# Kernel optimization log

Measured on AMD Instinct MI355X. Metric: run time of the kernel, lower is better.

## Reference

```python
import jax, jax.numpy as jnp
import numpy as np

D_MODEL = 1024
NUM_HEADS = 16
ENERGY_SCALE = 0.1
LN_EPS = 1e-5


def layernorm(x, gamma, beta):
    mu = jnp.mean(x, axis=-1, keepdims=True)
    var = jnp.var(x, axis=-1, keepdims=True)
    return (x - mu) * jax.lax.rsqrt(var + LN_EPS) * gamma + beta


def setup_inputs() -> dict:
    key = jax.random.key(0)
    ks = jax.random.split(key, 8)
    B, L, D = 2, 2048, D_MODEL
    s = 0.02
    return {
        "x": jax.random.normal(ks[0], (B, L, D), dtype=jnp.float32),
        "wq": jax.random.normal(ks[1], (D, D), dtype=jnp.float32) * s,
        "wk": jax.random.normal(ks[2], (D, D), dtype=jnp.float32) * s,
        "wv": jax.random.normal(ks[3], (D, D), dtype=jnp.float32) * s,
        "wo_w": jax.random.normal(ks[4], (D, D), dtype=jnp.float32) * s,
        "wo_b": jnp.zeros((D,), dtype=jnp.float32),
        "ep_w": jax.random.normal(ks[5], (D, D), dtype=jnp.float32) * s,
        "ep_b": jnp.zeros((D,), dtype=jnp.float32),
        "en_g": jnp.ones((D,), dtype=jnp.float32),
        "en_b": jnp.zeros((D,), dtype=jnp.float32),
        "ln_g": jnp.ones((D,), dtype=jnp.float32),
        "ln_b": jnp.zeros((D,), dtype=jnp.float32),
    }


def reference(x, wq, wk, wv, wo_w, wo_b, ep_w, ep_b, en_g, en_b, ln_g, ln_b):
    B, L, D = x.shape
    H, dk = NUM_HEADS, D // NUM_HEADS
    # Linear projections (torch convention: y = x @ W^T), split heads -> [B,H,L,dk]
    q = (x @ wq.T).reshape(B, L, H, dk).transpose(0, 2, 1, 3)
    k = (x @ wk.T).reshape(B, L, H, dk).transpose(0, 2, 1, 3)
    v = (x @ wv.T).reshape(B, L, H, dk).transpose(0, 2, 1, 3)
    scores = jnp.einsum("bhld,bhmd->bhlm", q, k) / jnp.sqrt(jnp.float32(dk))
    # Energy bias: ef @ ef^T as a proper GEMM (same math as the broadcast-mul-sum)
    ef = layernorm(x @ ep_w.T + ep_b, en_g, en_b)
    energy_bias = jnp.einsum("bld,bmd->blm", ef, ef)  # [B,L,L]
    scores = scores + ENERGY_SCALE * energy_bias[:, None, :, :]
    attn = jax.nn.softmax(scores, axis=-1)  # dropout is identity in eval mode
    ctx = jnp.einsum("bhlm,bhmd->bhld", attn, v)
    ctx = ctx.transpose(0, 2, 1, 3).reshape(B, L, D)
    out = ctx @ wo_w.T + wo_b
    return layernorm(out + x, ln_g, ln_b), attn
```

## Files before the change

kernel.cpp:

```cpp
#include <hip/hip_runtime.h>
#include <math.h>

#define D_MODEL 1024
#define NUM_HEADS 16
#define DK 64
#define L_SEQ 2048
#define BATCH 2
#define LN_EPS 1e-5f
#define ENERGY_SCALE 0.1f

typedef __attribute__((ext_vector_type(8))) short short8;
typedef __attribute__((ext_vector_type(4))) float f32x4;
typedef __attribute__((address_space(1))) const unsigned int gas_u32;
typedef __attribute__((address_space(3))) unsigned int las_u32;

__device__ __forceinline__ float waveReduceSum(float v) {
#pragma unroll
    for (int off = 32; off > 0; off >>= 1) v += __shfl_xor(v, off, 64);
    return v;
}

__device__ __forceinline__ unsigned short f2bf(float f) {
    unsigned int u = __float_as_uint(f);
    u += 0x7fff + ((u >> 16) & 1);
    return (unsigned short)(u >> 16);
}
__device__ __forceinline__ float bf2f(unsigned short u) {
    return __uint_as_float((unsigned int)u << 16);
}

__global__ __launch_bounds__(256) void cvt6(
    const float* s0, const float* s1, const float* s2,
    const float* s3, const float* s4, const float* s5,
    unsigned short* d0, unsigned short* d1, unsigned short* d2,
    unsigned short* d3, unsigned short* d4, unsigned short* d5,
    long long n0, long long n1, long long n2, long long n3, long long n4, long long n5)
{
    const float* s; unsigned short* d; long long n;
    switch (blockIdx.y) {
        case 0: s = s0; d = d0; n = n0; break;
        case 1: s = s1; d = d1; n = n1; break;
        case 2: s = s2; d = d2; n = n2; break;
        case 3: s = s3; d = d3; n = n3; break;
        case 4: s = s4; d = d4; n = n4; break;
        default: s = s5; d = d5; n = n5; break;
    }
    long long i = ((long long)blockIdx.x * 256 + threadIdx.x) * 4;
    if (i >= n) return;
    float4 v = *(const float4*)(s + i);
    ushort4 o;
    o.x = f2bf(v.x); o.y = f2bf(v.y); o.z = f2bf(v.z); o.w = f2bf(v.w);
    *(ushort4*)(d + i) = o;
}

__global__ __launch_bounds__(256) void gemm_bf16(
    const unsigned short* __restrict__ A, const unsigned short* __restrict__ B,
    const float* __restrict__ bias, float* __restrict__ Cf, unsigned short* __restrict__ Ch,
    int N, int K, long long sA, long long sB, long long sC)
{
    A += (long long)blockIdx.z * sA;
    B += (long long)blockIdx.z * sB;
    __shared__ unsigned short As[128 * 64];
    __shared__ unsigned short Bs[128 * 64];
    const int tid = threadIdx.x;
    const int lane = tid & 63, w = tid >> 6;
    const int quad = lane >> 4, col = lane & 15;
    const int wm = w & 1, wn = w >> 1;
    const int row0 = blockIdx.y * 128, col0 = blockIdx.x * 128;

    const int lr = lane >> 3, lc = lane & 7;
    const int gcs = (lc ^ lr) * 8;

    f32x4 acc[4][4];
#pragma unroll
    for (int mt = 0; mt < 4; mt++)
#pragma unroll
        for (int nt = 0; nt < 4; nt++) acc[mt][nt] = (f32x4){0.f, 0.f, 0.f, 0.f};

    for (int k0 = 0; k0 < K; k0 += 64) {
        __syncthreads();
#pragma unroll
        for (int p = 0; p < 4; p++) {
            const int rb = w * 32 + p * 8;
            __builtin_amdgcn_global_load_lds(
                (gas_u32*)(A + (long long)(row0 + rb + lr) * K + k0 + gcs),
                (las_u32*)(As + rb * 64), 16, 0, 0);
            __builtin_amdgcn_global_load_lds(
                (gas_u32*)(B + (long long)(col0 + rb + lr) * K + k0 + gcs),
                (las_u32*)(Bs + rb * 64), 16, 0, 0);
        }
        __syncthreads();
#pragma unroll
        for (int kc = 0; kc < 2; kc++) {
            const int csw = ((quad + 4 * kc) ^ (col & 7)) * 8;
            short8 af[4], bfr[4];
#pragma unroll
            for (int mt = 0; mt < 4; mt++)
                af[mt] = *(const short8*)(As + (wm * 64 + mt * 16 + col) * 64 + csw);
#pragma unroll
            for (int nt = 0; nt < 4; nt++)
                bfr[nt] = *(const short8*)(Bs + (wn * 64 + nt * 16 + col) * 64 + csw);
#pragma unroll
            for (int mt = 0; mt < 4; mt++)
#pragma unroll
                for (int nt = 0; nt < 4; nt++)
                    acc[mt][nt] = __builtin_amdgcn_mfma_f32_16x16x32_bf16(af[mt], bfr[nt], acc[mt][nt], 0, 0, 0);
        }
    }

#pragma unroll
    for (int mt = 0; mt < 4; mt++)
#pragma unroll
        for (int nt = 0; nt < 4; nt++)
#pragma unroll
            for (int reg = 0; reg < 4; reg++) {
                long long row = row0 + wm * 64 + mt * 16 + quad * 4 + reg;
                int c = col0 + wn * 64 + nt * 16 + col;
                float v = acc[mt][nt][reg];
                if (bias) v += bias[c];
                if (Cf) Cf[blockIdx.z * sC + row * N + c] = v;
                else    Ch[blockIdx.z * sC + row * N + c] = f2bf(v);
            }
}

__global__ __launch_bounds__(256) void proj_gemm(
    const unsigned short* __restrict__ Xh,
    const unsigned short* __restrict__ wqh, const unsigned short* __restrict__ wkh,
    const unsigned short* __restrict__ wvh, const unsigned short* __restrict__ eph,
    const float* __restrict__ ep_b,
    unsigned short* __restrict__ Qh, unsigned short* __restrict__ Kh,
    unsigned short* __restrict__ Vf, float* __restrict__ EP)
{
    const unsigned short* B;
    switch (blockIdx.z) {
        case 0: B = wqh; break;
        case 1: B = wkh; break;
        case 2: B = wvh; break;
        default: B = eph; break;
    }
    __shared__ unsigned short As[128 * 64];
    __shared__ unsigned short Bs[128 * 64];
    const int tid = threadIdx.x;
    const int lane = tid & 63, w = tid >> 6;
    const int quad = lane >> 4, col = lane & 15;
    const int wm = w & 1, wn = w >> 1;
    const int row0 = blockIdx.y * 128, col0 = blockIdx.x * 128;
    const int K = D_MODEL, N = D_MODEL;

    const int lr = lane >> 3, lc = lane & 7;
    const int gcs = (lc ^ lr) * 8;

    f32x4 acc[4][4];
#pragma unroll
    for (int mt = 0; mt < 4; mt++)
#pragma unroll
        for (int nt = 0; nt < 4; nt++) acc[mt][nt] = (f32x4){0.f, 0.f, 0.f, 0.f};

    for (int k0 = 0; k0 < K; k0 += 64) {
        __syncthreads();
#pragma unroll
        for (int p = 0; p < 4; p++) {
            const int rb = w * 32 + p * 8;
            __builtin_amdgcn_global_load_lds(
                (gas_u32*)(Xh + (long long)(row0 + rb + lr) * K + k0 + gcs),
                (las_u32*)(As + rb * 64), 16, 0, 0);
            __builtin_amdgcn_global_load_lds(
                (gas_u32*)(B + (long long)(col0 + rb + lr) * K + k0 + gcs),
                (las_u32*)(Bs + rb * 64), 16, 0, 0);
        }
        __syncthreads();
#pragma unroll
        for (int kc = 0; kc < 2; kc++) {
            const int csw = ((quad + 4 * kc) ^ (col & 7)) * 8;
            short8 af[4], bfr[4];
#pragma unroll
            for (int mt = 0; mt < 4; mt++)
                af[mt] = *(const short8*)(As + (wm * 64 + mt * 16 + col) * 64 + csw);
#pragma unroll
            for (int nt = 0; nt < 4; nt++)
                bfr[nt] = *(const short8*)(Bs + (wn * 64 + nt * 16 + col) * 64 + csw);
#pragma unroll
            for (int mt = 0; mt < 4; mt++)
#pragma unroll
                for (int nt = 0; nt < 4; nt++)
                    acc[mt][nt] = __builtin_amdgcn_mfma_f32_16x16x32_bf16(af[mt], bfr[nt], acc[mt][nt], 0, 0, 0);
        }
    }

    unsigned short* Hout = (blockIdx.z == 0) ? Qh : (blockIdx.z == 1) ? Kh : Vf;
#pragma unroll
    for (int mt = 0; mt < 4; mt++)
#pragma unroll
        for (int nt = 0; nt < 4; nt++)
#pragma unroll
            for (int reg = 0; reg < 4; reg++) {
                long long row = row0 + wm * 64 + mt * 16 + quad * 4 + reg;
                int c = col0 + wn * 64 + nt * 16 + col;
                float v = acc[mt][nt][reg];
                if (blockIdx.z == 3) EP[row * N + c] = v + ep_b[c];
                else                 Hout[row * N + c] = f2bf(v);
            }
}

__global__ __launch_bounds__(256) void ln_rows(
    const float* __restrict__ in, const float* __restrict__ res,
    const float* __restrict__ g, const float* __restrict__ bta,
    float* __restrict__ outf, unsigned short* __restrict__ outh)
{
    const long long row = blockIdx.x;
    const float* ip = in + row * D_MODEL;
    const float* rp = res ? res + row * D_MODEL : nullptr;
    const int tid = threadIdx.x;
    float vals[4];
    float s = 0.f, ss = 0.f;
#pragma unroll
    for (int j = 0; j < 4; j++) {
        int idx = tid + j * 256;
        float v = ip[idx];
        if (rp) v += rp[idx];
        vals[j] = v; s += v; ss += v * v;
    }
    __shared__ float sred[4], ssred[4];
    s = waveReduceSum(s); ss = waveReduceSum(ss);
    int wave = tid >> 6, lane = tid & 63;
    if (lane == 0) { sred[wave] = s; ssred[wave] = ss; }
    __syncthreads();
    float ts = sred[0] + sred[1] + sred[2] + sred[3];
    float tss = ssred[0] + ssred[1] + ssred[2] + ssred[3];
    float mu = ts * (1.f / D_MODEL);
    float var = tss * (1.f / D_MODEL) - mu * mu;
    float rs = rsqrtf(var + LN_EPS);
#pragma unroll
    for (int j = 0; j < 4; j++) {
        int idx = tid + j * 256;
        float o = (vals[j] - mu) * rs * g[idx] + bta[idx];
        if (outf) outf[row * D_MODEL + idx] = o;
        else      outh[row * D_MODEL + idx] = f2bf(o);
    }
}

__global__ __launch_bounds__(256) void transpose_v(
    const unsigned short* __restrict__ V, unsigned short* __restrict__ Vt)
{
    const int m0 = blockIdx.x * 64, h = blockIdx.y, b = blockIdx.z;
    __shared__ unsigned int t[64][65];
    const int tid = threadIdx.x;
    {
        int r = tid >> 4, c4 = (tid & 15) * 4;
#pragma unroll
        for (int i = 0; i < 4; i++) {
            int row = r + i * 16;
            ushort4 v = *(const ushort4*)(V + ((long long)b * L_SEQ + m0 + row) * D_MODEL + h * DK + c4);
            t[row][c4] = v.x; t[row][c4 + 1] = v.y; t[row][c4 + 2] = v.z; t[row][c4 + 3] = v.w;
        }
    }
    __syncthreads();
    const int lane = tid & 63, wv = tid >> 6;
#pragma unroll
    for (int i = 0; i < 16; i++) {
        int d = wv * 16 + i;
        Vt[(((long long)(b * NUM_HEADS + h)) * DK + d) * L_SEQ + m0 + lane] = (unsigned short)t[lane][d];
    }
}

__global__ __launch_bounds__(256) void eb_stats(
    const float* __restrict__ EB, float* __restrict__ ebmax, float* __restrict__ ebtmax)
{
    const long long row = blockIdx.x;
    const float* p = EB + row * L_SEQ;
    const int tid = threadIdx.x;
    float4 a = *(const float4*)(p + tid * 8);
    float4 c = *(const float4*)(p + tid * 8 + 4);
    float m = fmaxf(fmaxf(fmaxf(a.x, a.y), fmaxf(a.z, a.w)),
                    fmaxf(fmaxf(c.x, c.y), fmaxf(c.z, c.w)));
    m = fmaxf(m, __shfl_xor(m, 1, 64));
    m = fmaxf(m, __shfl_xor(m, 2, 64));
    m = fmaxf(m, __shfl_xor(m, 4, 64));
    if ((tid & 7) == 0) ebtmax[row * 32 + (tid >> 3)] = m;
    m = fmaxf(m, __shfl_xor(m, 8, 64));
    m = fmaxf(m, __shfl_xor(m, 16, 64));
    m = fmaxf(m, __shfl_xor(m, 32, 64));
    __shared__ float red[4];
    if ((tid & 63) == 0) red[tid >> 6] = m;
    __syncthreads();
    if (tid == 0)
        ebmax[row] = fmaxf(fmaxf(red[0], red[1]), fmaxf(red[2], red[3]));
}

__global__ __launch_bounds__(256) void qk_stats(
    const unsigned short* __restrict__ Qh, const unsigned short* __restrict__ Kh,
    float* __restrict__ qn, float* __restrict__ kn)
{
    const int l0 = blockIdx.x * 64, h = blockIdx.y, b = blockIdx.z;
    const int tid = threadIdx.x;
    const int r = tid >> 2, p4 = (tid & 3) * 16;
    const unsigned short* q = Qh + ((long long)b * L_SEQ + l0 + r) * D_MODEL + h * DK + p4;
    const unsigned short* k = Kh + ((long long)b * L_SEQ + l0 + r) * D_MODEL + h * DK + p4;
    float sq = 0.f, sk = 0.f;
#pragma unroll
    for (int i = 0; i < 16; i++) {
        float qv = bf2f(q[i]); sq += qv * qv;
        float kv = bf2f(k[i]); sk += kv * kv;
    }
    sq += __shfl_xor(sq, 1, 64); sq += __shfl_xor(sq, 2, 64);
    sk += __shfl_xor(sk, 1, 64); sk += __shfl_xor(sk, 2, 64);
    if ((tid & 3) == 0) {
        long long idx = ((long long)(b * NUM_HEADS + h)) * L_SEQ + l0 + r;
        qn[idx] = sqrtf(sq);
        kn[idx] = sqrtf(sk);
    }
}

__global__ __launch_bounds__(256) void kstats2(
    const float* __restrict__ kn, float* __restrict__ kmax, float* __restrict__ ktmax)
{
    const long long bh = blockIdx.x;
    const float* p = kn + bh * L_SEQ;
    const int tid = threadIdx.x;
    float4 a = *(const float4*)(p + tid * 8);
    float4 c = *(const float4*)(p + tid * 8 + 4);
    float m = fmaxf(fmaxf(fmaxf(a.x, a.y), fmaxf(a.z, a.w)),
                    fmaxf(fmaxf(c.x, c.y), fmaxf(c.z, c.w)));
    m = fmaxf(m, __shfl_xor(m, 1, 64));
    m = fmaxf(m, __shfl_xor(m, 2, 64));
    m = fmaxf(m, __shfl_xor(m, 4, 64));
    if ((tid & 7) == 0) ktmax[bh * 32 + (tid >> 3)] = m;
    m = fmaxf(m, __shfl_xor(m, 8, 64));
    m = fmaxf(m, __shfl_xor(m, 16, 64));
    m = fmaxf(m, __shfl_xor(m, 32, 64));
    __shared__ float red[4];
    if ((tid & 63) == 0) red[tid >> 6] = m;
    __syncthreads();
    if (tid == 0)
        kmax[bh] = fmaxf(fmaxf(red[0], red[1]), fmaxf(red[2], red[3]));
}

__global__ __launch_bounds__(64) void skip_mask(
    const float* __restrict__ ebmax, const float* __restrict__ ebtmax,
    const float* __restrict__ qn, const float* __restrict__ kmax,
    const float* __restrict__ ktmax, unsigned int* __restrict__ skipm)
{
    const int l0 = blockIdx.x * 64, h = blockIdx.y, b = blockIdx.z;
    const int tid = threadIdx.x;
    const int row = l0 + tid;
    const int bh = b * NUM_HEADS + h;
    float q = qn[(long long)bh * L_SEQ + row];
    float Mh = ENERGY_SCALE * ebmax[(long long)b * L_SEQ + row] + q * kmax[bh] * 0.125f + 0.02f;
    const float* ebt = ebtmax + ((long long)b * L_SEQ + row) * 32;
    const float* ktm = ktmax + bh * 32;
    unsigned int m = 0;
    for (int t = 0; t < 32; t++) {
        float ub = ENERGY_SCALE * ebt[t] + q * ktm[t] * 0.125f;
        unsigned long long bal = __ballot(ub < Mh - 45.0f);
        if (bal == ~0ull) m |= (1u << t);
    }
    if (tid == 0) skipm[bh * 32 + blockIdx.x] = m;
}

__global__ __launch_bounds__(256) void attn_mfma(
    const unsigned short* __restrict__ Qh, const unsigned short* __restrict__ Kh,
    const unsigned short* __restrict__ Vt, const float* __restrict__ EB,
    const float* __restrict__ ebmax, const float* __restrict__ qn,
    const float* __restrict__ kmax, const unsigned int* __restrict__ skipm,
    float* __restrict__ attn_out, unsigned short* __restrict__ CTXh)
{
    __shared__ unsigned short Ks[2][64 * 64];
    __shared__ unsigned short Vts[64 * 64];
    __shared__ unsigned short Ps[4 * 16 * 72];

    const int tid = threadIdx.x;
    const int lane = tid & 63, w = tid >> 6;
    const int quad = lane >> 4, col = lane & 15;
    const int l0 = blockIdx.x * 64;
    const int h = blockIdx.y, b = blockIdx.z;

    const unsigned int sm = skipm[(b * NUM_HEADS + h) * 32 + blockIdx.x];

    const unsigned short* kbase = Kh + ((long long)b * L_SEQ) * D_MODEL + h * DK;
    const unsigned short* vbase = Vt + ((long long)(b * NUM_HEADS + h)) * DK * L_SEQ;

    const int lr = lane >> 3, lc = lane & 7;
    const int gsw = (lc ^ lr) * 8;

    auto nxt = [&](int t) -> int {
        unsigned int rem = ~sm;
        if (t >= 0) rem &= (t >= 31) ? 0u : (0xFFFFFFFFu << (t + 1));
        return rem ? (int)__builtin_ctz(rem) : -1;
    };
    const int t0 = nxt(-1);

    if (t0 >= 0) {
#pragma unroll
        for (int p = 0; p < 2; p++) {
            const int rb = w * 8 + p * 32;
            __builtin_amdgcn_global_load_lds(
                (gas_u32*)(kbase + (long long)(t0 * 64 + rb + lr) * D_MODEL + gsw),
                (las_u32*)(&Ks[0][rb * 64]), 16, 0, 0);
        }
    }

    {
        float* zbase = attn_out + (((long long)(b * NUM_HEADS + h)) * L_SEQ + l0) * L_SEQ;
        const int zc = (tid & 15) * 4;
        const int zr = tid >> 4;
        const float4 zv = {0.f, 0.f, 0.f, 0.f};
        for (int t = 0; t < 32; t++) {
            if (!(sm & (1u << t))) continue;
            float* tb = zbase + t * 64 + zc;
#pragma unroll
            for (int rr = 0; rr < 4; rr++)
                *(float4*)(tb + (long long)(rr * 16 + zr) * L_SEQ) = zv;
        }
    }

    short8 aq[2];
    {
        const unsigned short* qrow = Qh + ((long long)b * L_SEQ + l0 + w * 16 + col) * D_MODEL + h * DK;
        aq[0] = *(const short8*)(qrow + quad * 8);
        aq[1] = *(const short8*)(qrow + 32 + quad * 8);
    }

    float Mhat[4];
    {
        const float km = kmax[b * NUM_HEADS + h];
#pragma unroll
        for (int reg = 0; reg < 4; reg++) {
            int row = l0 + w * 16 + quad * 4 + reg;
            float qb = qn[((long long)(b * NUM_HEADS + h)) * L_SEQ + row];
            Mhat[reg] = ENERGY_SCALE * ebmax[(long long)b * L_SEQ + row] +
                        qb * km * 0.125f + 0.02f;
        }
    }

    const float* ebp = EB + ((long long)b * L_SEQ + l0 + w * 16 + quad * 4) * L_SEQ + col;

    __syncthreads();

    float rowSacc[4] = {0.f, 0.f, 0.f, 0.f};
    int cur = 0;
    for (int t = t0; t >= 0; ) {
        const int tn = nxt(t);
        if (tn >= 0) {
#pragma unroll
            for (int p = 0; p < 2; p++) {
                const int rb = w * 8 + p * 32;
                __builtin_amdgcn_global_load_lds(
                    (gas_u32*)(kbase + (long long)(tn * 64 + rb + lr) * D_MODEL + gsw),
                    (las_u32*)(&Ks[cur ^ 1][rb * 64]), 16, 0, 0);
            }
        }
        const int m0 = t * 64;

        f32x4 acc[4];
#pragma unroll
        for (int nt = 0; nt < 4; nt++) acc[nt] = (f32x4){0.f, 0.f, 0.f, 0.f};
        __builtin_amdgcn_s_setprio(1);
#pragma unroll
        for (int nt = 0; nt < 4; nt++)
#pragma unroll
            for (int kc = 0; kc < 2; kc++) {
                short8 bk = *(const short8*)(&Ks[cur][((nt * 16 + col) << 6) +
                                                     (((quad + 4 * kc) ^ (col & 7)) << 3)]);
                acc[nt] = __builtin_amdgcn_mfma_f32_16x16x32_bf16(aq[kc], bk, acc[nt], 0, 0, 0);
            }
        __builtin_amdgcn_s_setprio(0);
#pragma unroll
        for (int nt = 0; nt < 4; nt++)
#pragma unroll
            for (int reg = 0; reg < 4; reg++) {
                float s = acc[nt][reg] * 0.125f + ENERGY_SCALE * ebp[(long long)reg * L_SEQ + m0 + nt * 16];
                rowSacc[reg] += __expf(s - Mhat[reg]);
            }
        __syncthreads();
        cur ^= 1;
        t = tn;
    }

    float invS[4];
#pragma unroll
    for (int reg = 0; reg < 4; reg++) {
        float v = rowSacc[reg];
#pragma unroll
        for (int off = 8; off > 0; off >>= 1) v += __shfl_xor(v, off, 64);
        invS[reg] = 1.f / v;
    }

    cur = 0;
    if (t0 >= 0) {
#pragma unroll
        for (int p = 0; p < 2; p++) {
            const int rb = w * 8 + p * 32;
            __builtin_amdgcn_global_load_lds(
                (gas_u32*)(kbase + (long long)(t0 * 64 + rb + lr) * D_MODEL + gsw),
                (las_u32*)(&Ks[0][rb * 64]), 16, 0, 0);
        }
    }
    __syncthreads();

    f32x4 ctx[4];
#pragma unroll
    for (int nt = 0; nt < 4; nt++) ctx[nt] = (f32x4){0.f, 0.f, 0.f, 0.f};

    unsigned short* Psw = Ps + w * 16 * 72;
    float* aob = attn_out + (((long long)(b * NUM_HEADS + h)) * L_SEQ + l0 + w * 16 + quad * 4) * L_SEQ + col;

    for (int t = t0; t >= 0; ) {
        const int tn = nxt(t);
        const int m0 = t * 64;

#pragma unroll
        for (int p = 0; p < 2; p++) {
            const int rb = w * 8 + p * 32;
            __builtin_amdgcn_global_load_lds(
                (gas_u32*)(vbase + (long long)(rb + lr) * L_SEQ + m0 + gsw),
                (las_u32*)(&Vts[rb * 64]), 16, 0, 0);
        }
        if (tn >= 0) {
#pragma unroll
            for (int p = 0; p < 2; p++) {
                const int rb = w * 8 + p * 32;
                __builtin_amdgcn_global_load_lds(
                    (gas_u32*)(kbase + (long long)(tn * 64 + rb + lr) * D_MODEL + gsw),
                    (las_u32*)(&Ks[cur ^ 1][rb * 64]), 16, 0, 0);
            }
        }

        f32x4 acc[4];
#pragma unroll
        for (int nt = 0; nt < 4; nt++) acc[nt] = (f32x4){0.f, 0.f, 0.f, 0.f};
        __builtin_amdgcn_s_setprio(1);
#pragma unroll
        for (int nt = 0; nt < 4; nt++)
#pragma unroll
            for (int kc = 0; kc < 2; kc++) {
                short8 bk = *(const short8*)(&Ks[cur][((nt * 16 + col) << 6) +
                                                     (((quad + 4 * kc) ^ (col & 7)) << 3)]);
                acc[nt] = __builtin_amdgcn_mfma_f32_16x16x32_bf16(aq[kc], bk, acc[nt], 0, 0, 0);
            }
        __builtin_amdgcn_s_setprio(0);

#pragma unroll
        for (int nt = 0; nt < 4; nt++)
#pragma unroll
            for (int reg = 0; reg < 4; reg++) {
                float s = acc[nt][reg] * 0.125f + ENERGY_SCALE * ebp[(long long)reg * L_SEQ + m0 + nt * 16];
                float p = __expf(s - Mhat[reg]) * invS[reg];
                acc[nt][reg] = p;
                Psw[(quad * 4 + reg) * 72 + nt * 16 + col] = f2bf(p);
            }
        __syncthreads();

#pragma unroll
        for (int nt = 0; nt < 4; nt++)
#pragma unroll
            for (int reg = 0; reg < 4; reg++)
                aob[(long long)reg * L_SEQ + m0 + nt * 16] = acc[nt][reg];

        short8 ap[2];
#pragma unroll
        for (int kc = 0; kc < 2; kc++)
            ap[kc] = *(const short8*)(Psw + col * 72 + quad * 8 + kc * 32);
        __builtin_amdgcn_s_setprio(1);
#pragma unroll
        for (int nt = 0; nt < 4; nt++)
#pragma unroll
            for (int kc = 0; kc < 2; kc++) {
                short8 bv = *(const short8*)(&Vts[((nt * 16 + col) << 6) +
                                                  (((quad + 4 * kc) ^ (col & 7)) << 3)]);
                ctx[nt] = __builtin_amdgcn_mfma_f32_16x16x32_bf16(ap[kc], bv, ctx[nt], 0, 0, 0);
            }
        __builtin_amdgcn_s_setprio(0);
        __syncthreads();
        cur ^= 1;
        t = tn;
    }

#pragma unroll
    for (int nt = 0; nt < 4; nt++)
#pragma unroll
        for (int reg = 0; reg < 4; reg++)
            CTXh[((long long)b * L_SEQ + l0 + w * 16 + quad * 4 + reg) * D_MODEL + h * DK + nt * 16 + col] =
                f2bf(ctx[nt][reg]);
}

extern "C" void kernel_launch(void* const* d_in, const int* in_sizes, int n_in,
                              void* d_out, int out_size, void* d_ws, size_t ws_size,
                              hipStream_t stream) {
    const float* x    = (const float*)d_in[0];
    const float* wq   = (const float*)d_in[1];
    const float* wk   = (const float*)d_in[2];
    const float* wv   = (const float*)d_in[3];
    const float* wo_w = (const float*)d_in[4];
    const float* wo_b = (const float*)d_in[5];
    const float* ep_w = (const float*)d_in[6];
    const float* ep_b = (const float*)d_in[7];
    const float* en_g = (const float*)d_in[8];
    const float* en_b = (const float*)d_in[9];
    const float* ln_g = (const float*)d_in[10];
    const float* ln_b = (const float*)d_in[11];

    float* out_final = (float*)d_out;
    float* attn_out  = out_final + (long long)BATCH * L_SEQ * D_MODEL;

    const long long MD = (long long)BATCH * L_SEQ * D_MODEL;
    const long long WN = (long long)D_MODEL * D_MODEL;
    const long long BH = (long long)BATCH * NUM_HEADS;

    float* EB = (float*)d_ws;
    float* EP = EB + (long long)BATCH * L_SEQ * L_SEQ;
    unsigned short* Xh   = (unsigned short*)(EP + MD);
    unsigned short* Qh   = Xh + MD;
    unsigned short* Kh   = Qh + MD;
    unsigned short* Vf   = Kh + MD;
    unsigned short* Vt   = Vf + MD;
    unsigned short* EFh  = Vt + MD;
    unsigned short* CTXh = EFh + MD;
    unsigned short* wqh  = CTXh + MD;
    unsigned short* wkh  = wqh + WN;
    unsigned short* wvh  = wkh + WN;
    unsigned short* eph  = wvh + WN;
    unsigned short* woh  = eph + WN;
    float* ebmax  = (float*)(woh + WN);
    float* qn     = ebmax + (long long)BATCH * L_SEQ;
    float* kn     = qn + BH * L_SEQ;
    float* kmax   = kn + BH * L_SEQ;
    float* ktmax  = kmax + BH;
    float* ebtmax = ktmax + BH * 32;
    unsigned int* skipm = (unsigned int*)(ebtmax + (long long)BATCH * L_SEQ * 32);
    float* OUT = EP;

    const int M = BATCH * L_SEQ;
    dim3 blk(256);

    cvt6<<<dim3((unsigned)(MD / 1024), 6), blk, 0, stream>>>(
        x, wq, wk, wv, ep_w, wo_w, Xh, wqh, wkh, wvh, eph, woh,
        MD, WN, WN, WN, WN, WN);

    proj_gemm<<<dim3(D_MODEL / 128, M / 128, 4), blk, 0, stream>>>(
        Xh, wqh, wkh, wvh, eph, ep_b, Qh, Kh, Vf, EP);

    ln_rows<<<dim3(M), blk, 0, stream>>>(EP, nullptr, en_g, en_b, nullptr, EFh);

    gemm_bf16<<<dim3(L_SEQ / 128, L_SEQ / 128, BATCH), blk, 0, stream>>>(
        EFh, EFh, nullptr, EB, nullptr, L_SEQ, D_MODEL,
        (long long)L_SEQ * D_MODEL, (long long)L_SEQ * D_MODEL,
        (long long)L_SEQ * L_SEQ);

    qk_stats<<<dim3(L_SEQ / 64, NUM_HEADS, BATCH), blk, 0, stream>>>(Qh, Kh, qn, kn);
    kstats2<<<dim3((unsigned)BH), blk, 0, stream>>>(kn, kmax, ktmax);
    eb_stats<<<dim3(M), blk, 0, stream>>>(EB, ebmax, ebtmax);
    skip_mask<<<dim3(L_SEQ / 64, NUM_HEADS, BATCH), dim3(64), 0, stream>>>(
        ebmax, ebtmax, qn, kmax, ktmax, skipm);

    transpose_v<<<dim3(L_SEQ / 64, NUM_HEADS, BATCH), blk, 0, stream>>>(Vf, Vt);

    attn_mfma<<<dim3(L_SEQ / 64, NUM_HEADS, BATCH), blk, 0, stream>>>(
        Qh, Kh, Vt, EB, ebmax, qn, kmax, skipm, attn_out, CTXh);

    gemm_bf16<<<dim3(D_MODEL / 128, M / 128, 1), blk, 0, stream>>>(
        CTXh, woh, wo_b, OUT, nullptr, D_MODEL, D_MODEL, 0, 0, 0);

    ln_rows<<<dim3(M), blk, 0, stream>>>(OUT, x, ln_g, ln_b, out_final, nullptr);
}
```

Measured before the change: 752.8 us.

## Store energy bias in bf16 and drop the tile skip-mask machinery

The energy-bias matrix is now written by the GEMM and read by the stats and attention kernels as bf16 instead of fp32, which halves its footprint and memory traffic. At the same time the per-tile upper-bound skip mask is removed: the skip_mask kernel, the ebtmax/ktmax tile maxima, and the zero-fill of skipped attention tiles are deleted. Every key tile is now always processed in both softmax passes. This gives up a data-dependent shortcut that likely skipped most tiles, because the diagonal energy term dominates. It also adds bf16 rounding error to large bias values that feed the exponent.

```diff
diff --git a/kernel.cpp b/kernel.cpp
--- a/kernel.cpp
+++ b/kernel.cpp
@@ -264,22 +264,17 @@
 }
 
 __global__ __launch_bounds__(256) void eb_stats(
-    const float* __restrict__ EB, float* __restrict__ ebmax, float* __restrict__ ebtmax)
+    const unsigned short* __restrict__ EBh, float* __restrict__ ebmax)
 {
     const long long row = blockIdx.x;
-    const float* p = EB + row * L_SEQ;
-    const int tid = threadIdx.x;
-    float4 a = *(const float4*)(p + tid * 8);
-    float4 c = *(const float4*)(p + tid * 8 + 4);
-    float m = fmaxf(fmaxf(fmaxf(a.x, a.y), fmaxf(a.z, a.w)),
-                    fmaxf(fmaxf(c.x, c.y), fmaxf(c.z, c.w)));
-    m = fmaxf(m, __shfl_xor(m, 1, 64));
-    m = fmaxf(m, __shfl_xor(m, 2, 64));
-    m = fmaxf(m, __shfl_xor(m, 4, 64));
-    if ((tid & 7) == 0) ebtmax[row * 32 + (tid >> 3)] = m;
-    m = fmaxf(m, __shfl_xor(m, 8, 64));
-    m = fmaxf(m, __shfl_xor(m, 16, 64));
-    m = fmaxf(m, __shfl_xor(m, 32, 64));
+    const unsigned short* p = EBh + row * L_SEQ;
+    const int tid = threadIdx.x;
+    short8 v = *(const short8*)(p + tid * 8);
+    float m = bf2f((unsigned short)v[0]);
+#pragma unroll
+    for (int j = 1; j < 8; j++) m = fmaxf(m, bf2f((unsigned short)v[j]));
+#pragma unroll
+    for (int off = 32; off > 0; off >>= 1) m = fmaxf(m, __shfl_xor(m, off, 64));
     __shared__ float red[4];
     if ((tid & 63) == 0) red[tid >> 6] = m;
     __syncthreads();
@@ -312,7 +307,7 @@
 }
 
 __global__ __launch_bounds__(256) void kstats2(
-    const float* __restrict__ kn, float* __restrict__ kmax, float* __restrict__ ktmax)
+    const float* __restrict__ kn, float* __restrict__ kmax)
 {
     const long long bh = blockIdx.x;
     const float* p = kn + bh * L_SEQ;
@@ -321,13 +316,8 @@
     float4 c = *(const float4*)(p + tid * 8 + 4);
     float m = fmaxf(fmaxf(fmaxf(a.x, a.y), fmaxf(a.z, a.w)),
                     fmaxf(fmaxf(c.x, c.y), fmaxf(c.z, c.w)));
-    m = fmaxf(m, __shfl_xor(m, 1, 64));
-    m = fmaxf(m, __shfl_xor(m, 2, 64));
-    m = fmaxf(m, __shfl_xor(m, 4, 64));
-    if ((tid & 7) == 0) ktmax[bh * 32 + (tid >> 3)] = m;
-    m = fmaxf(m, __shfl_xor(m, 8, 64));
-    m = fmaxf(m, __shfl_xor(m, 16, 64));
-    m = fmaxf(m, __shfl_xor(m, 32, 64));
+#pragma unroll
+    for (int off = 32; off > 0; off >>= 1) m = fmaxf(m, __shfl_xor(m, off, 64));
     __shared__ float red[4];
     if ((tid & 63) == 0) red[tid >> 6] = m;
     __syncthreads();
@@ -335,33 +325,11 @@
         kmax[bh] = fmaxf(fmaxf(red[0], red[1]), fmaxf(red[2], red[3]));
 }
 
-__global__ __launch_bounds__(64) void skip_mask(
-    const float* __restrict__ ebmax, const float* __restrict__ ebtmax,
-    const float* __restrict__ qn, const float* __restrict__ kmax,
-    const float* __restrict__ ktmax, unsigned int* __restrict__ skipm)
-{
-    const int l0 = blockIdx.x * 64, h = blockIdx.y, b = blockIdx.z;
-    const int tid = threadIdx.x;
-    const int row = l0 + tid;
-    const int bh = b * NUM_HEADS + h;
-    float q = qn[(long long)bh * L_SEQ + row];
-    float Mh = ENERGY_SCALE * ebmax[(long long)b * L_SEQ + row] + q * kmax[bh] * 0.125f + 0.02f;
-    const float* ebt = ebtmax + ((long long)b * L_SEQ + row) * 32;
-    const float* ktm = ktmax + bh * 32;
-    unsigned int m = 0;
-    for (int t = 0; t < 32; t++) {
-        float ub = ENERGY_SCALE * ebt[t] + q * ktm[t] * 0.125f;
-        unsigned long long bal = __ballot(ub < Mh - 45.0f);
-        if (bal == ~0ull) m |= (1u << t);
-    }
-    if (tid == 0) skipm[bh * 32 + blockIdx.x] = m;
-}
-
 __global__ __launch_bounds__(256) void attn_mfma(
     const unsigned short* __restrict__ Qh, const unsigned short* __restrict__ Kh,
-    const unsigned short* __restrict__ Vt, const float* __restrict__ EB,
+    const unsigned short* __restrict__ Vt, const unsigned short* __restrict__ EBh,
     const float* __restrict__ ebmax, const float* __restrict__ qn,
-    const float* __restrict__ kmax, const unsigned int* __restrict__ skipm,
+    const float* __restrict__ kmax,
     float* __restrict__ attn_out, unsigned short* __restrict__ CTXh)
 {
     __shared__ unsigned short Ks[2][64 * 64];
@@ -374,43 +342,18 @@
     const int l0 = blockIdx.x * 64;
     const int h = blockIdx.y, b = blockIdx.z;
 
-    const unsigned int sm = skipm[(b * NUM_HEADS + h) * 32 + blockIdx.x];
-
     const unsigned short* kbase = Kh + ((long long)b * L_SEQ) * D_MODEL + h * DK;
     const unsigned short* vbase = Vt + ((long long)(b * NUM_HEADS + h)) * DK * L_SEQ;
 
     const int lr = lane >> 3, lc = lane & 7;
     const int gsw = (lc ^ lr) * 8;
 
-    auto nxt = [&](int t) -> int {
-        unsigned int rem = ~sm;
-        if (t >= 0) rem &= (t >= 31) ? 0u : (0xFFFFFFFFu << (t + 1));
-        return rem ? (int)__builtin_ctz(rem) : -1;
-    };
-    const int t0 = nxt(-1);
-
-    if (t0 >= 0) {
-#pragma unroll
-        for (int p = 0; p < 2; p++) {
-            const int rb = w * 8 + p * 32;
-            __builtin_amdgcn_global_load_lds(
-                (gas_u32*)(kbase + (long long)(t0 * 64 + rb + lr) * D_MODEL + gsw),
-                (las_u32*)(&Ks[0][rb * 64]), 16, 0, 0);
-        }
-    }
-
-    {
-        float* zbase = attn_out + (((long long)(b * NUM_HEADS + h)) * L_SEQ + l0) * L_SEQ;
-        const int zc = (tid & 15) * 4;
-        const int zr = tid >> 4;
-        const float4 zv = {0.f, 0.f, 0.f, 0.f};
-        for (int t = 0; t < 32; t++) {
-            if (!(sm & (1u << t))) continue;
-            float* tb = zbase + t * 64 + zc;
-#pragma unroll
-            for (int rr = 0; rr < 4; rr++)
-                *(float4*)(tb + (long long)(rr * 16 + zr) * L_SEQ) = zv;
-        }
+#pragma unroll
+    for (int p = 0; p < 2; p++) {
+        const int rb = w * 8 + p * 32;
+        __builtin_amdgcn_global_load_lds(
+            (gas_u32*)(kbase + (long long)(rb + lr) * D_MODEL + gsw),
+            (las_u32*)(&Ks[0][rb * 64]), 16, 0, 0);
     }
 
     short8 aq[2];
@@ -432,20 +375,19 @@
         }
     }
 
-    const float* ebp = EB + ((long long)b * L_SEQ + l0 + w * 16 + quad * 4) * L_SEQ + col;
+    const unsigned short* ebp = EBh + ((long long)b * L_SEQ + l0 + w * 16 + quad * 4) * L_SEQ + col;
 
     __syncthreads();
 
     float rowSacc[4] = {0.f, 0.f, 0.f, 0.f};
     int cur = 0;
-    for (int t = t0; t >= 0; ) {
-        const int tn = nxt(t);
-        if (tn >= 0) {
+    for (int t = 0; t < 32; t++) {
+        if (t < 31) {
 #pragma unroll
             for (int p = 0; p < 2; p++) {
                 const int rb = w * 8 + p * 32;
                 __builtin_amdgcn_global_load_lds(
-                    (gas_u32*)(kbase + (long long)(tn * 64 + rb + lr) * D_MODEL + gsw),
+                    (gas_u32*)(kbase + (long long)((t + 1) * 64 + rb + lr) * D_MODEL + gsw),
                     (las_u32*)(&Ks[cur ^ 1][rb * 64]), 16, 0, 0);
             }
         }
@@ -468,12 +410,12 @@
         for (int nt = 0; nt < 4; nt++)
 #pragma unroll
             for (int reg = 0; reg < 4; reg++) {
-                float s = acc[nt][reg] * 0.125f + ENERGY_SCALE * ebp[(long long)reg * L_SEQ + m0 + nt * 16];
+                float e = bf2f(ebp[(long long)reg * L_SEQ + m0 + nt * 16]);
+                float s = acc[nt][reg] * 0.125f + ENERGY_SCALE * e;
                 rowSacc[reg] += __expf(s - Mhat[reg]);
             }
         __syncthreads();
         cur ^= 1;
-        t = tn;
     }
 
     float invS[4];
@@ -486,14 +428,12 @@
     }
 
     cur = 0;
-    if (t0 >= 0) {
-#pragma unroll
-        for (int p = 0; p < 2; p++) {
-            const int rb = w * 8 + p * 32;
-            __builtin_amdgcn_global_load_lds(
-                (gas_u32*)(kbase + (long long)(t0 * 64 + rb + lr) * D_MODEL + gsw),
-                (las_u32*)(&Ks[0][rb * 64]), 16, 0, 0);
-        }
+#pragma unroll
+    for (int p = 0; p < 2; p++) {
+        const int rb = w * 8 + p * 32;
+        __builtin_amdgcn_global_load_lds(
+            (gas_u32*)(kbase + (long long)(rb + lr) * D_MODEL + gsw),
+            (las_u32*)(&Ks[0][rb * 64]), 16, 0, 0);
     }
     __syncthreads();
 
@@ -504,8 +444,7 @@
     unsigned short* Psw = Ps + w * 16 * 72;
     float* aob = attn_out + (((long long)(b * NUM_HEADS + h)) * L_SEQ + l0 + w * 16 + quad * 4) * L_SEQ + col;
 
-    for (int t = t0; t >= 0; ) {
-        const int tn = nxt(t);
+    for (int t = 0; t < 32; t++) {
         const int m0 = t * 64;
 
 #pragma unroll
@@ -515,12 +454,12 @@
                 (gas_u32*)(vbase + (long long)(rb + lr) * L_SEQ + m0 + gsw),
                 (las_u32*)(&Vts[rb * 64]), 16, 0, 0);
         }
-        if (tn >= 0) {
+        if (t < 31) {
 #pragma unroll
             for (int p = 0; p < 2; p++) {
                 const int rb = w * 8 + p * 32;
                 __builtin_amdgcn_global_load_lds(
-                    (gas_u32*)(kbase + (long long)(tn * 64 + rb + lr) * D_MODEL + gsw),
+                    (gas_u32*)(kbase + (long long)((t + 1) * 64 + rb + lr) * D_MODEL + gsw),
                     (las_u32*)(&Ks[cur ^ 1][rb * 64]), 16, 0, 0);
             }
         }
@@ -543,7 +482,8 @@
         for (int nt = 0; nt < 4; nt++)
 #pragma unroll
             for (int reg = 0; reg < 4; reg++) {
-                float s = acc[nt][reg] * 0.125f + ENERGY_SCALE * ebp[(long long)reg * L_SEQ + m0 + nt * 16];
+                float e = bf2f(ebp[(long long)reg * L_SEQ + m0 + nt * 16]);
+                float s = acc[nt][reg] * 0.125f + ENERGY_SCALE * e;
                 float p = __expf(s - Mhat[reg]) * invS[reg];
                 acc[nt][reg] = p;
                 Psw[(quad * 4 + reg) * 72 + nt * 16 + col] = f2bf(p);
@@ -572,7 +512,6 @@
         __builtin_amdgcn_s_setprio(0);
         __syncthreads();
         cur ^= 1;
-        t = tn;
     }
 
 #pragma unroll
@@ -605,9 +544,10 @@
     const long long MD = (long long)BATCH * L_SEQ * D_MODEL;
     const long long WN = (long long)D_MODEL * D_MODEL;
     const long long BH = (long long)BATCH * NUM_HEADS;
-
-    float* EB = (float*)d_ws;
-    float* EP = EB + (long long)BATCH * L_SEQ * L_SEQ;
+    const long long LL = (long long)BATCH * L_SEQ * L_SEQ;
+
+    unsigned short* EBh = (unsigned short*)d_ws;
+    float* EP = (float*)(EBh + LL);
     unsigned short* Xh   = (unsigned short*)(EP + MD);
     unsigned short* Qh   = Xh + MD;
     unsigned short* Kh   = Qh + MD;
@@ -624,9 +564,6 @@
     float* qn     = ebmax + (long long)BATCH * L_SEQ;
     float* kn     = qn + BH * L_SEQ;
     float* kmax   = kn + BH * L_SEQ;
-    float* ktmax  = kmax + BH;
-    float* ebtmax = ktmax + BH * 32;
-    unsigned int* skipm = (unsigned int*)(ebtmax + (long long)BATCH * L_SEQ * 32);
     float* OUT = EP;
 
     const int M = BATCH * L_SEQ;
@@ -642,20 +579,18 @@
     ln_rows<<<dim3(M), blk, 0, stream>>>(EP, nullptr, en_g, en_b, nullptr, EFh);
 
     gemm_bf16<<<dim3(L_SEQ / 128, L_SEQ / 128, BATCH), blk, 0, stream>>>(
-        EFh, EFh, nullptr, EB, nullptr, L_SEQ, D_MODEL,
+        EFh, EFh, nullptr, nullptr, EBh, L_SEQ, D_MODEL,
         (long long)L_SEQ * D_MODEL, (long long)L_SEQ * D_MODEL,
         (long long)L_SEQ * L_SEQ);
 
     qk_stats<<<dim3(L_SEQ / 64, NUM_HEADS, BATCH), blk, 0, stream>>>(Qh, Kh, qn, kn);
-    kstats2<<<dim3((unsigned)BH), blk, 0, stream>>>(kn, kmax, ktmax);
-    eb_stats<<<dim3(M), blk, 0, stream>>>(EB, ebmax, ebtmax);
-    skip_mask<<<dim3(L_SEQ / 64, NUM_HEADS, BATCH), dim3(64), 0, stream>>>(
-        ebmax, ebtmax, qn, kmax, ktmax, skipm);
+    kstats2<<<dim3((unsigned)BH), blk, 0, stream>>>(kn, kmax);
+    eb_stats<<<dim3(M), blk, 0, stream>>>(EBh, ebmax);
 
     transpose_v<<<dim3(L_SEQ / 64, NUM_HEADS, BATCH), blk, 0, stream>>>(Vf, Vt);
 
     attn_mfma<<<dim3(L_SEQ / 64, NUM_HEADS, BATCH), blk, 0, stream>>>(
-        Qh, Kh, Vt, EB, ebmax, qn, kmax, skipm, attn_out, CTXh);
+        Qh, Kh, Vt, EBh, ebmax, qn, kmax, attn_out, CTXh);
 
     gemm_bf16<<<dim3(D_MODEL / 128, M / 128, 1), blk, 0, stream>>>(
         CTXh, woh, wo_b, OUT, nullptr, D_MODEL, D_MODEL, 0, 0, 0);
```

After: 930.3 us. +23.6%, slower.
